# Performance work log

Measured on AMD Instinct MI355X. Metric: run time of the kernel, lower is better.

Reference implementation:

```python
import jax, jax.numpy as jnp
import numpy as np
import math

N = 12288
IN_MAIN, IN_MOD = 64, 128
NC_INNER, NC_QK, OUT_MAIN = 16, 8, 64

def setup_inputs() -> dict:
    key = jax.random.key(0)
    ks = jax.random.split(key, 8)
    s = lambda fan_in: 1.0 / np.sqrt(fan_in)
    return {
        "x_main": jax.random.normal(ks[0], (N, IN_MAIN), dtype=jnp.float32),
        "x_mod": jax.random.normal(ks[1], (N, IN_MOD), dtype=jnp.float32),
        "xyz": jax.random.uniform(ks[2], (N, 3), dtype=jnp.float32),
        # MLP E: [in_main+in_mod -> nc_inner -> nc_inner], bias=False (weights stored [in, out])
        "W_e1": jax.random.uniform(ks[3], (IN_MAIN + IN_MOD, NC_INNER), jnp.float32, -s(IN_MAIN + IN_MOD), s(IN_MAIN + IN_MOD)),
        "W_e2": jax.random.uniform(ks[4], (NC_INNER, NC_INNER), jnp.float32, -s(NC_INNER), s(NC_INNER)),
        "W_q": jax.random.uniform(ks[5], (NC_INNER, NC_QK), jnp.float32, -s(NC_INNER), s(NC_INNER)),
        "W_k": jax.random.uniform(ks[6], (NC_INNER, NC_QK), jnp.float32, -s(NC_INNER), s(NC_INNER)),
        "W_v": jax.random.uniform(ks[7], (NC_INNER, OUT_MAIN), jnp.float32, -s(NC_INNER), s(NC_INNER)),
    }

def reference(x_main, x_mod, xyz, W_e1, W_e2, W_q, W_k, W_v):
    # concat 3D + 2D features: [N, in_main+in_mod]
    x = jnp.concatenate((x_main, x_mod), axis=-1)
    # MLP E (bias-free Linear + ReLU per layer): [N, nc_inner]
    h = jax.nn.relu(jax.nn.relu(x @ W_e1) @ W_e2)
    Q = h @ W_q  # [N, nc_qk]
    K = h @ W_k  # [N, nc_qk]
    V = h @ W_v  # [N, out_main]
    scale = 1.0 / math.sqrt(NC_QK)
    scores = (Q @ K.T) * scale          # [N, N] full global attention
    attn = jax.nn.softmax(scores, axis=1)
    return attn @ V                     # [N, out_main]
```

## Files before the change

kernel.cpp:

```cpp
#include <hip/hip_runtime.h>
#include <stdint.h>


#define NN 12288

typedef float    f32x16 __attribute__((ext_vector_type(16)));
typedef short    s16x8  __attribute__((ext_vector_type(8)));
typedef unsigned short u16;

#define MFMA_32x32x16_BF16 __builtin_amdgcn_mfma_f32_32x32x16_bf16

#define OFF_QB   0u
#define OFF_VT   196608u
#define OFF_PO   2162688u

#define WC_VM(n)   (0x0F70 | (n))
#define WC_LGKM0   (0xC07F)

typedef __attribute__((address_space(3))) void lds_void_t;
typedef const __attribute__((address_space(1))) void gbl_void_t;
__device__ __forceinline__ void gld16(const void* g, void* l) {
    __builtin_amdgcn_global_load_lds((gbl_void_t*)g, (lds_void_t*)l, 16, 0, 0);
}

__device__ __forceinline__ float bf2f(u16 s) {
    union { unsigned int u; float f; } c; c.u = ((unsigned int)s) << 16; return c.f;
}
__device__ __forceinline__ u16 f2bf(float f) {
    union { float f; unsigned int u; } c; c.f = f;
    return (u16)((c.u + 0x8000u) >> 16);
}
__device__ __forceinline__ unsigned int pk2(float a, float b) {
    union { float f; unsigned int u; } ca, cb; ca.f = a; cb.f = b;
    return ((ca.u + 0x8000u) >> 16) | ((cb.u + 0x8000u) & 0xffff0000u);
}
__device__ __forceinline__ unsigned int pkbf(float a, float b) {
#if __has_builtin(__builtin_amdgcn_cvt_pk_bf16_f32)
    auto r = __builtin_amdgcn_cvt_pk_bf16_f32(a, b);
    union { decltype(r) v; unsigned int u; } c; c.v = r; return c.u;
#else
    return pk2(a, b);
#endif
}
__device__ __forceinline__ f32x16 zf16() {
    f32x16 z;
#pragma unroll
    for (int i = 0; i < 16; ++i) z[i] = 0.f;
    return z;
}
__device__ __forceinline__ s16x8 zs8() {
    s16x8 z;
#pragma unroll
    for (int i = 0; i < 8; ++i) z[i] = 0;
    return z;
}

union U8 { s16x8 v; unsigned int u[4]; };
union QV { uint4 q; s16x8 v; };

__global__ __launch_bounds__(256) void k1_qkv(
    const void* __restrict__ xmain, const void* __restrict__ xmod,
    const void* __restrict__ we1, const void* __restrict__ we2,
    const void* __restrict__ wqp, const void* __restrict__ wkp,
    const void* __restrict__ wvp,
    u16* __restrict__ qb, u16* __restrict__ vt)
{
    __shared__ float wf[4608];
    __shared__ int   sflag;
    __shared__ float lh1[64][4][17];
    __shared__ float lh2[64][17];

    const int t = threadIdx.x;
    const int r = t >> 2;
    const int p = t & 3;
    const int row = blockIdx.x * 64 + r;

    if (t == 0) sflag = 0;
    __syncthreads();
    {
        float v = bf2f(((const u16*)xmod)[2 * t]);
        if (fabsf(v) > 16.f) atomicAdd(&sflag, 1);
    }
    __syncthreads();
    const int isf32 = (sflag > 8);

    const float SCL = 0.51006979f;
    if (isf32) {
        const float* a1 = (const float*)we1; const float* a2 = (const float*)we2;
        const float* aq = (const float*)wqp; const float* ak = (const float*)wkp;
        const float* av = (const float*)wvp;
        for (int i = t; i < 4608; i += 256) {
            if      (i < 3072) wf[i] = a1[i];
            else if (i < 3328) wf[i] = a2[i - 3072];
            else if (i < 3456) wf[i] = aq[i - 3328] * SCL;
            else if (i < 3584) wf[i] = ak[i - 3456];
            else               wf[i] = av[i - 3584];
        }
    } else {
        const u16* a1 = (const u16*)we1; const u16* a2 = (const u16*)we2;
        const u16* aq = (const u16*)wqp; const u16* ak = (const u16*)wkp;
        const u16* av = (const u16*)wvp;
        for (int i = t; i < 4608; i += 256) {
            if      (i < 3072) wf[i] = bf2f(a1[i]);
            else if (i < 3328) wf[i] = bf2f(a2[i - 3072]);
            else if (i < 3456) wf[i] = bf2f(aq[i - 3328]) * SCL;
            else if (i < 3584) wf[i] = bf2f(ak[i - 3456]);
            else               wf[i] = bf2f(av[i - 3584]);
        }
    }
    __syncthreads();

    const float* __restrict__ W1 = wf;
    const float* __restrict__ W2 = wf + 3072;
    const float* __restrict__ Wq = wf + 3328;
    const float* __restrict__ Wk = wf + 3456;
    const float* __restrict__ Wv = wf + 3584;

    float h1p[16];
#pragma unroll
    for (int o = 0; o < 16; ++o) h1p[o] = 0.f;

    if (isf32) {
#pragma unroll
        for (int cc = 0; cc < 12; ++cc) {
            const int c = p + cc * 4;
            float4 xv = (c < 16)
                ? ((const float4*)xmain)[(size_t)row * 16 + c]
                : ((const float4*)xmod)[(size_t)row * 32 + (c - 16)];
            float xs[4] = {xv.x, xv.y, xv.z, xv.w};
#pragma unroll
            for (int j = 0; j < 4; ++j) {
                const float* wr = W1 + (c * 4 + j) * 16;
#pragma unroll
                for (int o = 0; o < 16; ++o) h1p[o] += xs[j] * wr[o];
            }
        }
    } else {
#pragma unroll
        for (int cc = 0; cc < 12; ++cc) {
            const int c = p + cc * 4;
            uint2 xv = (c < 16)
                ? ((const uint2*)xmain)[(size_t)row * 16 + c]
                : ((const uint2*)xmod)[(size_t)row * 32 + (c - 16)];
            float xs[4] = { bf2f((u16)(xv.x & 0xffff)), bf2f((u16)(xv.x >> 16)),
                            bf2f((u16)(xv.y & 0xffff)), bf2f((u16)(xv.y >> 16)) };
#pragma unroll
            for (int j = 0; j < 4; ++j) {
                const float* wr = W1 + (c * 4 + j) * 16;
#pragma unroll
                for (int o = 0; o < 16; ++o) h1p[o] += xs[j] * wr[o];
            }
        }
    }
#pragma unroll
    for (int o = 0; o < 16; ++o) lh1[r][p][o] = h1p[o];
    __syncthreads();

    float h1[16];
#pragma unroll
    for (int o = 0; o < 16; ++o)
        h1[o] = fmaxf(lh1[r][0][o] + lh1[r][1][o] + lh1[r][2][o] + lh1[r][3][o], 0.f);

#pragma unroll
    for (int oo = 0; oo < 4; ++oo) {
        const int o = p * 4 + oo;
        float s = 0.f;
#pragma unroll
        for (int j = 0; j < 16; ++j) s += h1[j] * W2[j * 16 + o];
        lh2[r][o] = fmaxf(s, 0.f);
    }
    __syncthreads();

    float h2[16];
#pragma unroll
    for (int j = 0; j < 16; ++j) h2[j] = lh2[r][j];

    const int tt = row >> 5, kk = row & 31;
    {
        float q0 = 0.f, q1 = 0.f, k0 = 0.f, k1 = 0.f;
        const int o = 2 * p;
#pragma unroll
        for (int j = 0; j < 16; ++j) {
            q0 += h2[j] * Wq[j * 8 + o];
            q1 += h2[j] * Wq[j * 8 + o + 1];
            k0 += h2[j] * Wk[j * 8 + o];
            k1 += h2[j] * Wk[j * 8 + o + 1];
        }
        ((unsigned int*)qb)[(size_t)row * 4 + p] = pk2(q0, q1);
        ((unsigned int*)vt)[(size_t)tt * 1152 + 1024 + kk * 4 + p] = pk2(k0, k1);
    }

    {
        const int b   = kk >> 4, kk4 = kk & 15;
        const int hh  = (kk4 >> 2) & 1;
        const int jj  = (kk4 & 3) + 4 * (kk4 >> 3);
        const size_t cbase = (size_t)tt * 2304 + b * 512 + hh * 256 + jj;
#pragma unroll
        for (int c16 = 0; c16 < 16; ++c16) {
            const int c = p * 16 + c16;
            float v = 0.f;
#pragma unroll
            for (int j = 0; j < 16; ++j) v += h2[j] * Wv[j * 64 + c];
            vt[cbase + (size_t)(c >> 5) * 1024 + (c & 31) * 8] = f2bf(v);
        }
    }
}


__global__ __launch_bounds__(256, 3) void k2_attn(
    const u16* __restrict__ qb, const u16* __restrict__ vt,
    u16* __restrict__ po, float* __restrict__ pl,
    int nsplit, int ntile)
{
    __shared__ uint4 smem[2304];

    const int tid  = threadIdx.x;
    const int lane = tid & 63;
    const int half = lane >> 5;
    const int l31  = lane & 31;
    const int w    = tid >> 6;
    const int qB   = (blockIdx.x % 96) * 128;
    const int sp   = blockIdx.x / 96;
    const int myq  = qB + 32 * w;
    const int tile0 = sp * (NN / nsplit) / 32;

    uint4* lb0 = &smem[w * 576];
    uint4* lb1 = lb0 + 288;

    const f32x16 Z = zf16();
    s16x8 qf = zs8();
    if (!half) qf = *(const s16x8*)(qb + (size_t)(myq + l31) * 8);

    s16x8 ones;
#pragma unroll
    for (int i = 0; i < 8; ++i) ones[i] = (short)0x3F80;

    f32x16 acc0 = Z, acc1 = Z, accl = Z;

#define STAGE(t, lbase) do {                                                  \
    const char* g_ = (const char*)vt + (size_t)(t) * 4608 + lane * 16;        \
    char* l_ = (char*)(lbase);                                                \
    gld16(g_, l_);                                                            \
    gld16(g_ + 1024, l_ + 1024);                                              \
    gld16(g_ + 2048, l_ + 2048);                                              \
    gld16(g_ + 3072, l_ + 3072);                                              \
    if (lane < 32) gld16(g_ + 4096, l_ + 4096);                               \
} while (0)

#define LDSK(lbase, ka) do {                                                  \
    (ka).q = *((const uint4*)(lbase) + 256 + l31);                            \
} while (0)

#define FIN(S_, lbase) do {                                                   \
    float pr_[16];                                                            \
    _Pragma("unroll")                                                         \
    for (int r_ = 0; r_ < 16; ++r_) pr_[r_] = __builtin_amdgcn_exp2f((S_)[r_]);\
    U8 p0_, p1_;                                                              \
    _Pragma("unroll")                                                         \
    for (int i_ = 0; i_ < 4; ++i_) {                                          \
        p0_.u[i_] = pkbf(pr_[2 * i_],     pr_[2 * i_ + 1]);                   \
        p1_.u[i_] = pkbf(pr_[8 + 2 * i_], pr_[8 + 2 * i_ + 1]);               \
    }                                                                         \
    accl = MFMA_32x32x16_BF16(ones, p0_.v, accl, 0, 0, 0);                    \
    accl = MFMA_32x32x16_BF16(ones, p1_.v, accl, 0, 0, 0);                    \
    QV f_;                                                                    \
    f_.q = *((const uint4*)(lbase) + lane);                                   \
    acc0 = MFMA_32x32x16_BF16(f_.v, p0_.v, acc0, 0, 0, 0);                    \
    f_.q = *((const uint4*)(lbase) + 128 + lane);                             \
    acc1 = MFMA_32x32x16_BF16(f_.v, p0_.v, acc1, 0, 0, 0);                    \
    f_.q = *((const uint4*)(lbase) + 64 + lane);                              \
    acc0 = MFMA_32x32x16_BF16(f_.v, p1_.v, acc0, 0, 0, 0);                    \
    f_.q = *((const uint4*)(lbase) + 192 + lane);                             \
    acc1 = MFMA_32x32x16_BF16(f_.v, p1_.v, acc1, 0, 0, 0);                    \
} while (0)

#define WAIT_VM(n) do {                                                       \
    __builtin_amdgcn_s_waitcnt(WC_VM(n));                                     \
    __builtin_amdgcn_sched_barrier(0);                                        \
} while (0)
#define WAIT_LGKM() do {                                                      \
    __builtin_amdgcn_s_waitcnt(WC_LGKM0);                                     \
    __builtin_amdgcn_sched_barrier(0);                                        \
} while (0)

    STAGE(tile0 + 0, lb0);
    STAGE(tile0 + 1, lb1);
    WAIT_VM(5);
    QV ka;
    LDSK(lb0, ka);
    f32x16 SA = MFMA_32x32x16_BF16(ka.v, qf, Z, 0, 0, 0);
    f32x16 SB;

    int gt = 0;
    for (; gt + 2 < ntile; gt += 2) {
        WAIT_VM(0);
        LDSK(lb1, ka);
        SB = MFMA_32x32x16_BF16(ka.v, qf, Z, 0, 0, 0);
        FIN(SA, lb0);
        WAIT_LGKM();
        STAGE(tile0 + gt + 2, lb0);
        WAIT_VM(0);
        LDSK(lb0, ka);
        SA = MFMA_32x32x16_BF16(ka.v, qf, Z, 0, 0, 0);
        FIN(SB, lb1);
        WAIT_LGKM();
        if (gt + 3 < ntile) STAGE(tile0 + gt + 3, lb1);
    }
    WAIT_VM(0);
    LDSK(lb1, ka);
    SB = MFMA_32x32x16_BF16(ka.v, qf, Z, 0, 0, 0);
    FIN(SA, lb0);
    FIN(SB, lb1);

#undef STAGE
#undef LDSK
#undef FIN
#undef WAIT_VM
#undef WAIT_LGKM

    const float ls = accl[0];

    WAIT_LGKM_EPI:;
    __builtin_amdgcn_s_waitcnt(WC_LGKM0);
    float* sfw = (float*)&smem[w * 576];
#pragma unroll
    for (int r = 0; r < 16; ++r) {
        const int c = (r & 3) + 8 * (r >> 2) + 4 * half;
        sfw[c * 33 + l31]        = acc0[r];
        sfw[(32 + c) * 33 + l31] = acc1[r];
    }
    if (lane < 32) sfw[2112 + l31] = ls;

    u16* poS = po + (size_t)sp * (NN * 64);
    const int lq  = lane >> 1;
    const int cb0 = (lane & 1) * 32;
    unsigned int u[16];
#pragma unroll
    for (int i = 0; i < 16; ++i)
        u[i] = pkbf(sfw[(cb0 + 2 * i) * 33 + lq],
                    sfw[(cb0 + 2 * i + 1) * 33 + lq]);
    u16* dst = poS + (size_t)(myq + lq) * 64 + cb0;
    *(uint4*)(dst)      = make_uint4(u[0],  u[1],  u[2],  u[3]);
    *(uint4*)(dst + 8)  = make_uint4(u[4],  u[5],  u[6],  u[7]);
    *(uint4*)(dst + 16) = make_uint4(u[8],  u[9],  u[10], u[11]);
    *(uint4*)(dst + 24) = make_uint4(u[12], u[13], u[14], u[15]);
    if (lane < 32)
        pl[(size_t)sp * NN + myq + l31] = sfw[2112 + l31];
}

__global__ __launch_bounds__(256) void k3_norm(
    const u16* __restrict__ po, const float* __restrict__ pl,
    float4* __restrict__ out, int nsplit)
{
    const int i = blockIdx.x * 256 + threadIdx.x;
    const int row = i >> 4;
    const int c0 = (i & 15) * 4;
    float l = 0.f;
    float o0 = 0.f, o1 = 0.f, o2 = 0.f, o3 = 0.f;
    for (int s = 0; s < nsplit; ++s) {
        l += pl[(size_t)s * NN + row];
        uint2 p = *(const uint2*)(po + (size_t)s * (NN * 64) +
                                  (size_t)row * 64 + c0);
        o0 += bf2f((u16)(p.x & 0xffff)); o1 += bf2f((u16)(p.x >> 16));
        o2 += bf2f((u16)(p.y & 0xffff)); o3 += bf2f((u16)(p.y >> 16));
    }
    const float rl = 1.0f / l;
    out[i] = make_float4(o0 * rl, o1 * rl, o2 * rl, o3 * rl);
}

extern "C" void kernel_launch(void* const* d_in, const int* in_sizes, int n_in,
                              void* d_out, int out_size, void* d_ws, size_t ws_size,
                              hipStream_t stream)
{
    const void* xmain = d_in[0];
    const void* xmod  = d_in[1];
    const void* we1   = d_in[3];
    const void* we2   = d_in[4];
    const void* wq    = d_in[5];
    const void* wk    = d_in[6];
    const void* wv    = d_in[7];

    char* ws = (char*)d_ws;
    u16*   qb   = (u16*)  (ws + OFF_QB);
    u16*   vt   = (u16*)  (ws + OFF_VT);

    int S = 8;
    while (S > 1) {
        size_t need = (size_t)OFF_PO + (size_t)S * (NN * 64 * 2) +
                      (size_t)S * (NN * 4);
        if (ws_size >= need) break;
        S >>= 1;
    }
    u16*   po = (u16*)(ws + OFF_PO);
    float* pl = (float*)(ws + OFF_PO + (size_t)S * (NN * 64 * 2));
    const int ntile = NN / (32 * S);

    k1_qkv<<<192, 256, 0, stream>>>(xmain, xmod, we1, we2, wq, wk, wv,
                                    qb, vt);
    k2_attn<<<96 * S, 256, 0, stream>>>(qb, vt, po, pl, S, ntile);
    k3_norm<<<768, 256, 0, stream>>>(po, pl, (float4*)d_out, S);
}
```

Measured before the change: 135.1 us.

## Split K into its own buffer and load it directly to registers

K is moved out of the interleaved V/K tile layout into a separate row-major buffer. The attention kernel now loads K tiles straight from global memory into registers two tiles ahead, while only V goes through LDS via global_load_lds. Waits become partial (vmcnt 6) instead of full drains, so the score MFMA no longer has to wait on an LDS round trip for K. The cost is more register pressure, and the loop needs a longer explicit epilogue that assumes ntile is at least 4.

New measurement: 132.6 us. Within noise of the previous version (-1.8%).

```diff
diff --git a/kernel.cpp b/kernel.cpp
--- a/kernel.cpp
+++ b/kernel.cpp
@@ -11,7 +11,8 @@
 #define MFMA_32x32x16_BF16 __builtin_amdgcn_mfma_f32_32x32x16_bf16
 
 #define OFF_QB   0u
-#define OFF_VT   196608u
+#define OFF_KB   196608u
+#define OFF_VT   393216u
 #define OFF_PO   2162688u
 
 #define WC_VM(n)   (0x0F70 | (n))
@@ -63,7 +64,7 @@
     const void* __restrict__ we1, const void* __restrict__ we2,
     const void* __restrict__ wqp, const void* __restrict__ wkp,
     const void* __restrict__ wvp,
-    u16* __restrict__ qb, u16* __restrict__ vt)
+    u16* __restrict__ qb, u16* __restrict__ kb, u16* __restrict__ vt)
 {
     __shared__ float wf[4608];
     __shared__ int   sflag;
@@ -187,14 +188,14 @@
             k1 += h2[j] * Wk[j * 8 + o + 1];
         }
         ((unsigned int*)qb)[(size_t)row * 4 + p] = pk2(q0, q1);
-        ((unsigned int*)vt)[(size_t)tt * 1152 + 1024 + kk * 4 + p] = pk2(k0, k1);
+        ((unsigned int*)kb)[(size_t)row * 4 + p] = pk2(k0, k1);
     }
 
     {
         const int b   = kk >> 4, kk4 = kk & 15;
         const int hh  = (kk4 >> 2) & 1;
         const int jj  = (kk4 & 3) + 4 * (kk4 >> 3);
-        const size_t cbase = (size_t)tt * 2304 + b * 512 + hh * 256 + jj;
+        const size_t cbase = (size_t)tt * 2048 + b * 512 + hh * 256 + jj;
 #pragma unroll
         for (int c16 = 0; c16 < 16; ++c16) {
             const int c = p * 16 + c16;
@@ -208,11 +209,12 @@
 
 
 __global__ __launch_bounds__(256, 3) void k2_attn(
-    const u16* __restrict__ qb, const u16* __restrict__ vt,
+    const u16* __restrict__ qb, const u16* __restrict__ kb,
+    const u16* __restrict__ vt,
     u16* __restrict__ po, float* __restrict__ pl,
     int nsplit, int ntile)
 {
-    __shared__ uint4 smem[2304];
+    __shared__ char smem[34816];
 
     const int tid  = threadIdx.x;
     const int lane = tid & 63;
@@ -224,8 +226,9 @@
     const int myq  = qB + 32 * w;
     const int tile0 = sp * (NN / nsplit) / 32;
 
-    uint4* lb0 = &smem[w * 576];
-    uint4* lb1 = lb0 + 288;
+    char* wbase = smem + w * 8704;
+    uint4* vb0 = (uint4*)wbase;
+    uint4* vb1 = vb0 + 256;
 
     const f32x16 Z = zf16();
     s16x8 qf = zs8();
@@ -238,17 +241,16 @@
     f32x16 acc0 = Z, acc1 = Z, accl = Z;
 
 #define STAGE(t, lbase) do {                                                  \
-    const char* g_ = (const char*)vt + (size_t)(t) * 4608 + lane * 16;        \
+    const char* g_ = (const char*)vt + (size_t)(t) * 4096 + lane * 16;        \
     char* l_ = (char*)(lbase);                                                \
     gld16(g_, l_);                                                            \
     gld16(g_ + 1024, l_ + 1024);                                              \
     gld16(g_ + 2048, l_ + 2048);                                              \
     gld16(g_ + 3072, l_ + 3072);                                              \
-    if (lane < 32) gld16(g_ + 4096, l_ + 4096);                               \
 } while (0)
 
-#define LDSK(lbase, ka) do {                                                  \
-    (ka).q = *((const uint4*)(lbase) + 256 + l31);                            \
+#define KLOAD(t, kr) do {                                                     \
+    (kr).q = *(const uint4*)(kb + (size_t)((tile0 + (t)) * 32 + l31) * 8);    \
 } while (0)
 
 #define FIN(S_, lbase) do {                                                   \
@@ -283,46 +285,58 @@
     __builtin_amdgcn_sched_barrier(0);                                        \
 } while (0)
 
-    STAGE(tile0 + 0, lb0);
-    STAGE(tile0 + 1, lb1);
-    WAIT_VM(5);
-    QV ka;
-    LDSK(lb0, ka);
-    f32x16 SA = MFMA_32x32x16_BF16(ka.v, qf, Z, 0, 0, 0);
+    QV krA, krB;
+    KLOAD(0, krA);
+    KLOAD(1, krB);
+    STAGE(tile0 + 0, vb0);
+    STAGE(tile0 + 1, vb1);
+    f32x16 SA = MFMA_32x32x16_BF16(krA.v, qf, Z, 0, 0, 0);
     f32x16 SB;
+    KLOAD(2, krA);
 
     int gt = 0;
-    for (; gt + 2 < ntile; gt += 2) {
-        WAIT_VM(0);
-        LDSK(lb1, ka);
-        SB = MFMA_32x32x16_BF16(ka.v, qf, Z, 0, 0, 0);
-        FIN(SA, lb0);
+    for (; gt + 6 <= ntile; gt += 2) {
+        SB = MFMA_32x32x16_BF16(krB.v, qf, Z, 0, 0, 0);
+        KLOAD(gt + 3, krB);
+        WAIT_VM(6);
+        FIN(SA, vb0);
         WAIT_LGKM();
-        STAGE(tile0 + gt + 2, lb0);
-        WAIT_VM(0);
-        LDSK(lb0, ka);
-        SA = MFMA_32x32x16_BF16(ka.v, qf, Z, 0, 0, 0);
-        FIN(SB, lb1);
+        STAGE(tile0 + gt + 2, vb0);
+        SA = MFMA_32x32x16_BF16(krA.v, qf, Z, 0, 0, 0);
+        WAIT_VM(6);
+        FIN(SB, vb1);
         WAIT_LGKM();
-        if (gt + 3 < ntile) STAGE(tile0 + gt + 3, lb1);
-    }
+        STAGE(tile0 + gt + 3, vb1);
+        KLOAD(gt + 4, krA);
+    }
+    SB = MFMA_32x32x16_BF16(krB.v, qf, Z, 0, 0, 0);
+    KLOAD(gt + 3, krB);
+    WAIT_VM(6);
+    FIN(SA, vb0);
+    WAIT_LGKM();
+    STAGE(tile0 + gt + 2, vb0);
+    SA = MFMA_32x32x16_BF16(krA.v, qf, Z, 0, 0, 0);
+    WAIT_VM(6);
+    FIN(SB, vb1);
+    WAIT_LGKM();
+    STAGE(tile0 + gt + 3, vb1);
+    SB = MFMA_32x32x16_BF16(krB.v, qf, Z, 0, 0, 0);
+    WAIT_VM(4);
+    FIN(SA, vb0);
     WAIT_VM(0);
-    LDSK(lb1, ka);
-    SB = MFMA_32x32x16_BF16(ka.v, qf, Z, 0, 0, 0);
-    FIN(SA, lb0);
-    FIN(SB, lb1);
+    FIN(SB, vb1);
 
 #undef STAGE
-#undef LDSK
+#undef KLOAD
 #undef FIN
 #undef WAIT_VM
 #undef WAIT_LGKM
 
     const float ls = accl[0];
 
-    WAIT_LGKM_EPI:;
     __builtin_amdgcn_s_waitcnt(WC_LGKM0);
-    float* sfw = (float*)&smem[w * 576];
+    __builtin_amdgcn_sched_barrier(0);
+    float* sfw = (float*)wbase;
 #pragma unroll
     for (int r = 0; r < 16; ++r) {
         const int c = (r & 3) + 8 * (r >> 2) + 4 * half;
@@ -382,6 +396,7 @@
 
     char* ws = (char*)d_ws;
     u16*   qb   = (u16*)  (ws + OFF_QB);
+    u16*   kb   = (u16*)  (ws + OFF_KB);
     u16*   vt   = (u16*)  (ws + OFF_VT);
 
     int S = 8;
@@ -396,7 +411,7 @@
     const int ntile = NN / (32 * S);
 
     k1_qkv<<<192, 256, 0, stream>>>(xmain, xmod, we1, we2, wq, wk, wv,
-                                    qb, vt);
-    k2_attn<<<96 * S, 256, 0, stream>>>(qb, vt, po, pl, S, ntile);
+                                    qb, kb, vt);
+    k2_attn<<<96 * S, 256, 0, stream>>>(qb, kb, vt, po, pl, S, ntile);
     k3_norm<<<768, 256, 0, stream>>>(po, pl, (float4*)d_out, S);
 }
```
